# Performance work log

Measured on AMD Instinct MI355X. Metric: run time of the kernel, lower is better.

Reference implementation:

```python
import jax, jax.numpy as jnp
import numpy as np

B, S, D, H, HD = 2, 2048, 2048, 16, 128
MAX_TIMESCALE = 10000.0


def _fixed_pos_embedding(features, length, max_timescale):
    # flaxformer embedding.generate_fixed_pos_embedding
    fraction = jnp.arange(0, features, 2, dtype=jnp.float32) / features
    timescale = max_timescale ** fraction  # min_timescale = 1.0
    sinusoid = jnp.einsum('i,j->ij', jnp.arange(length, dtype=jnp.float32), 1.0 / timescale)
    sinusoid = jnp.concatenate([sinusoid, sinusoid], axis=-1)  # [length, features]
    return jnp.sin(sinusoid), jnp.cos(sinusoid)


def _rotate_half(x):
    x1, x2 = jnp.split(x, 2, axis=-1)
    return jnp.concatenate([-x2, x1], axis=-1)


def _apply_rope(x, sin, cos):
    # x: [B, S, H, HD]; sin/cos: [S, HD]
    sin = sin[None, :, None, :].astype(x.dtype)
    cos = cos[None, :, None, :].astype(x.dtype)
    return x * cos + _rotate_half(x) * sin


def setup_inputs() -> dict:
    key = jax.random.key(0)
    ks = jax.random.split(key, 6)
    inputs_q = jax.random.normal(ks[0], (B, S, D), dtype=jnp.float32)
    inputs_kv = jax.random.normal(ks[1], (B, S, D), dtype=jnp.float32)
    scale = D ** -0.5
    wq = jax.random.normal(ks[2], (D, H, HD), dtype=jnp.float32) * scale
    wk = jax.random.normal(ks[3], (D, H, HD), dtype=jnp.float32) * scale
    wv = jax.random.normal(ks[4], (D, H, HD), dtype=jnp.float32) * scale
    wo = jax.random.normal(ks[5], (H, HD, D), dtype=jnp.float32) * ((H * HD) ** -0.5)
    mask = jnp.tril(jnp.ones((S, S), dtype=bool))[None, None]  # causal [1,1,S,S]
    return {"inputs_q": inputs_q, "inputs_kv": inputs_kv, "wq": wq, "wk": wk,
            "wv": wv, "wo": wo, "mask": mask}


def reference(inputs_q, inputs_kv, wq, wk, wv, wo, mask):
    # QKV projections (split-head kernels) -> [B, S, H, HD]
    q = jnp.einsum('bqd,dhf->bqhf', inputs_q, wq)
    k = jnp.einsum('bkd,dhf->bkhf', inputs_kv, wk)
    v = jnp.einsum('bkd,dhf->bkhf', inputs_kv, wv)

    # Rotary embeddings applied to full head dim (fraction_to_rotate = 1.0)
    sin, cos = _fixed_pos_embedding(HD, S, MAX_TIMESCALE)
    q = _apply_rope(q, sin, cos)
    k = _apply_rope(k, sin, cos)

    # Logit rescaling by 1/sqrt(head_dim) (rescale_logits=False default path)
    q = q * (HD ** -0.5)

    logits = jnp.einsum('bqhf,bkhf->bhqk', q, k)  # [B, H, S, S]
    logits = jnp.where(mask, logits, jnp.asarray(-1e10, logits.dtype))
    probs = jax.nn.softmax(logits, axis=-1)

    ctx = jnp.einsum('bhqk,bkhf->bqhf', probs, v)
    out = jnp.einsum('bqhf,hfd->bqd', ctx, wo)  # output projection
    return out
```

## Files before the change

kernel.cpp:

```cpp
#include <hip/hip_runtime.h>

#define S_LEN 2048
#define NH 16
#define HDIM 128
#define DMODEL 2048

typedef __attribute__((ext_vector_type(8))) short bf16x8;
typedef __attribute__((ext_vector_type(4))) float f32x4;

using gas_cvp = const __attribute__((address_space(1))) void*;
using las_vp  = __attribute__((address_space(3))) void*;

__device__ __forceinline__ unsigned short f2bf(float x) {
  unsigned int u = __builtin_bit_cast(unsigned int, x);
  u += 0x7FFFu + ((u >> 16) & 1u);
  return (unsigned short)(u >> 16);
}
__device__ __forceinline__ float bf2f(unsigned short u) {
  unsigned int x = ((unsigned int)u) << 16;
  return __builtin_bit_cast(float, x);
}
__device__ __forceinline__ unsigned int cvt_pk_bf16(float lo, float hi) {
  unsigned int r;
  asm("v_cvt_pk_bf16_f32 %0, %1, %2" : "=v"(r) : "v"(lo), "v"(hi));
  return r;
}

__global__ __launch_bounds__(256) void cvt_kernel(const float4* __restrict__ in,
                                                  ushort4* __restrict__ out, int n4) {
  int i = blockIdx.x * 256 + threadIdx.x;
  if (i < n4) {
    float4 v = in[i];
    ushort4 r;
    r.x = f2bf(v.x); r.y = f2bf(v.y); r.z = f2bf(v.z); r.w = f2bf(v.w);
    out[i] = r;
  }
}

__global__ __launch_bounds__(256) void sincos_kernel(float2* __restrict__ sc) {
  int i = blockIdx.x * 256 + threadIdx.x;
  int s = i >> 6, j = i & 63;
  float inv_ts = 1.0f / powf(10000.0f, (float)j * (1.0f / 64.0f));
  float ang = (float)s * inv_ts;
  sc[i] = make_float2(sinf(ang), cosf(ang));
}

__global__ __launch_bounds__(256) void rope8_kernel(const unsigned short* __restrict__ X,
                                                    const float2* __restrict__ sc,
                                                    unsigned short* __restrict__ out,
                                                    float scale) {
  int i = blockIdx.x * 256 + threadIdx.x;
  int m = i >> 7;
  int r = i & 127;
  int h = r >> 3, jb = (r & 7) * 8;
  int s = m & (S_LEN - 1);
  size_t base = (size_t)m * DMODEL + h * HDIM + jb;
  int4 x1 = *(const int4*)(X + base);
  int4 x2 = *(const int4*)(X + base + 64);
  const float2* pp = sc + s * 64 + jb;
  int4 o1, o2;
  int* x1w = (int*)&x1; int* x2w = (int*)&x2;
  int* o1w = (int*)&o1; int* o2w = (int*)&o2;
#pragma unroll
  for (int w = 0; w < 4; w++) {
    float a_lo = bf2f((unsigned short)(x1w[w] & 0xffff));
    float a_hi = bf2f((unsigned short)((unsigned int)x1w[w] >> 16));
    float b_lo = bf2f((unsigned short)(x2w[w] & 0xffff));
    float b_hi = bf2f((unsigned short)((unsigned int)x2w[w] >> 16));
    float2 c0 = pp[w * 2], c1 = pp[w * 2 + 1];
    float r1l = (a_lo * c0.y - b_lo * c0.x) * scale;
    float r1h = (a_hi * c1.y - b_hi * c1.x) * scale;
    float r2l = (b_lo * c0.y + a_lo * c0.x) * scale;
    float r2h = (b_hi * c1.y + a_hi * c1.x) * scale;
    o1w[w] = (int)(cvt_pk_bf16(r1l, r1h));
    o2w[w] = (int)(cvt_pk_bf16(r2l, r2h));
  }
  *(int4*)(out + base) = o1;
  *(int4*)(out + base + 64) = o2;
}

__global__ __launch_bounds__(256) void wtrans_kernel(const float* __restrict__ in,
                                                     unsigned short* __restrict__ out) {
  __shared__ float tile[64][65];
  int c0 = blockIdx.x * 64, r0 = blockIdx.y * 64;
  int tx = threadIdx.x & 63, ty = threadIdx.x >> 6;
#pragma unroll
  for (int i = 0; i < 16; i++) {
    int r = ty + i * 4;
    tile[r][tx] = in[(size_t)(r0 + r) * DMODEL + c0 + tx];
  }
  __syncthreads();
#pragma unroll
  for (int i = 0; i < 16; i++) {
    int c = ty + i * 4;
    out[(size_t)(c0 + c) * DMODEL + r0 + tx] = f2bf(tile[tx][c]);
  }
}

__global__ __launch_bounds__(256) void vtrans_kernel(const unsigned short* __restrict__ vf,
                                                     unsigned short* __restrict__ Vt) {
  __shared__ unsigned short tile[64][65];
  int z = blockIdx.z; int b = z >> 4, h = z & 15;
  const unsigned short* I = vf + (size_t)b * S_LEN * DMODEL + h * HDIM;
  unsigned short* O = Vt + (size_t)z * HDIM * S_LEN;
  int s0 = blockIdx.y * 64, f0 = blockIdx.x * 64;
  int tx = threadIdx.x & 63, ty = threadIdx.x >> 6;
#pragma unroll
  for (int i = 0; i < 16; i++) {
    int r = ty + i * 4;
    tile[r][tx] = I[(size_t)(s0 + r) * DMODEL + f0 + tx];
  }
  __syncthreads();
#pragma unroll
  for (int i = 0; i < 16; i++) {
    int c = ty + i * 4;
    O[(size_t)(f0 + c) * S_LEN + s0 + tx] = tile[tx][c];
  }
}

template <bool BF16OUT>
__global__ __launch_bounds__(512) void gemm4_kernel(
    const unsigned short* __restrict__ Aq,
    const unsigned short* __restrict__ Akv,
    const unsigned short* __restrict__ W,
    void* __restrict__ Cb) {
  constexpr int M = 4096, N = 2048, K = 2048, NT = K / 64;
  __shared__ char lds[98304];
  int z = blockIdx.z;
  const unsigned short* A = (z == 0) ? Aq : Akv;
  const unsigned short* Bt = W + (size_t)z * N * K;
  int bm = blockIdx.y * 256, bn = blockIdx.x * 128;
  int tid = threadIdx.x, wave = tid >> 6, lane = tid & 63;
  int lr = lane & 15, lq = lane >> 4;
  int wr = wave >> 1, wc = wave & 1;

  auto STAGE_U = [&](int t, int buf, int which) {
    int k0 = (t & (NT - 1)) * 64;
    const unsigned short* src = (which < 2) ? A : Bt;
    int rbase = (which < 2) ? (bm + which * 128) : bn;
    char* dst0 = lds + buf * 49152 + which * 16384;
#pragma unroll
    for (int i = 0; i < 2; i++) {
      int o = i * 8192 + wave * 1024 + lane * 16;
      int row = o >> 7, colb = o & 127;
      int sc = colb ^ ((row & 7) << 4);
      __builtin_amdgcn_global_load_lds(
          (gas_cvp)(src + (size_t)(rbase + row) * K + k0 + (sc >> 1)),
          (las_vp)(dst0 + i * 8192 + wave * 1024), 16, 0, 0);
    }
  };
  auto LDA = [&](int buf, int m, int kk) -> bf16x8 {
    int row = wr * 64 + m * 16 + lr;
    int half = row >> 7, r = row & 127;
    int byt = r * 128 + (((kk * 4 + lq) ^ (r & 7)) << 4);
    return *(const bf16x8*)(lds + buf * 49152 + half * 16384 + byt);
  };
  auto LDB = [&](int buf, int n, int kk) -> bf16x8 {
    int row = wc * 64 + n * 16 + lr;
    int byt = row * 128 + (((kk * 4 + lq) ^ (row & 7)) << 4);
    return *(const bf16x8*)(lds + buf * 49152 + 32768 + byt);
  };

  f32x4 acc[4][4] = {};
  bf16x8 aA[2][2], bB[4][2];

  auto MFMA_H = [&](int mg) {
#pragma unroll
    for (int kk = 0; kk < 2; kk++)
#pragma unroll
      for (int mm = 0; mm < 2; mm++)
#pragma unroll
        for (int nn = 0; nn < 4; nn++)
          acc[mg * 2 + mm][nn] = __builtin_amdgcn_mfma_f32_16x16x32_bf16(
              aA[mm][kk], bB[nn][kk], acc[mg * 2 + mm][nn], 0, 0, 0);
  };
  auto PHASE_SYNC = [&]() {
    __builtin_amdgcn_s_barrier();
    asm volatile("s_waitcnt lgkmcnt(0)" ::: "memory");
    __builtin_amdgcn_sched_barrier(0);
    __builtin_amdgcn_s_setprio(1);
  };
  auto PHASE_END = [&]() {
    __builtin_amdgcn_s_setprio(0);
    __builtin_amdgcn_s_barrier();
  };

  STAGE_U(0, 0, 0); STAGE_U(0, 0, 1); STAGE_U(0, 0, 2);
  asm volatile("s_waitcnt vmcnt(0)" ::: "memory");
  __builtin_amdgcn_sched_barrier(0);
  __builtin_amdgcn_s_barrier();

  for (int i = 0; i < NT / 2; i++) {
    int T1 = 2 * i + 1, TN = 2 * i + 2;
#pragma unroll
    for (int kk = 0; kk < 2; kk++) {
#pragma unroll
      for (int mm = 0; mm < 2; mm++) aA[mm][kk] = LDA(0, mm, kk);
#pragma unroll
      for (int nn = 0; nn < 4; nn++) bB[nn][kk] = LDB(0, nn, kk);
    }
    STAGE_U(T1, 1, 2); STAGE_U(T1, 1, 0);
    PHASE_SYNC(); MFMA_H(0); PHASE_END();

#pragma unroll
    for (int kk = 0; kk < 2; kk++)
#pragma unroll
      for (int mm = 0; mm < 2; mm++) aA[mm][kk] = LDA(0, 2 + mm, kk);
    STAGE_U(T1, 1, 1); STAGE_U(TN, 0, 2);
    asm volatile("s_waitcnt vmcnt(2)" ::: "memory");
    __builtin_amdgcn_sched_barrier(0);
    PHASE_SYNC(); MFMA_H(1); PHASE_END();

#pragma unroll
    for (int kk = 0; kk < 2; kk++) {
#pragma unroll
      for (int mm = 0; mm < 2; mm++) aA[mm][kk] = LDA(1, mm, kk);
#pragma unroll
      for (int nn = 0; nn < 4; nn++) bB[nn][kk] = LDB(1, nn, kk);
    }
    STAGE_U(TN, 0, 0); STAGE_U(TN, 0, 1);
    PHASE_SYNC(); MFMA_H(0); PHASE_END();

#pragma unroll
    for (int kk = 0; kk < 2; kk++)
#pragma unroll
      for (int mm = 0; mm < 2; mm++) aA[mm][kk] = LDA(1, 2 + mm, kk);
    asm volatile("s_waitcnt vmcnt(0)" ::: "memory");
    __builtin_amdgcn_sched_barrier(0);
    PHASE_SYNC(); MFMA_H(1); PHASE_END();
  }

#pragma unroll
  for (int m = 0; m < 4; m++)
#pragma unroll
    for (int n = 0; n < 4; n++) {
      int row0 = bm + wr * 64 + m * 16 + lq * 4;
      int col = bn + wc * 64 + n * 16 + lr;
      if (BF16OUT) {
        unsigned short* C = (unsigned short*)Cb + (size_t)z * M * N;
#pragma unroll
        for (int r = 0; r < 4; r++)
          C[(size_t)(row0 + r) * N + col] = f2bf(acc[m][n][r]);
      } else {
        float* C = (float*)Cb + (size_t)z * M * N;
#pragma unroll
        for (int r = 0; r < 4; r++)
          C[(size_t)(row0 + r) * N + col] = acc[m][n][r];
      }
    }
}

__global__ __launch_bounds__(512, 1) void attn_kernel(const unsigned short* __restrict__ Qb,
                                                      const unsigned short* __restrict__ Kb,
                                                      const unsigned short* __restrict__ Vt,
                                                      unsigned short* __restrict__ ctx) {
  __shared__ char lds[65536];
  int b = blockIdx.z, h = blockIdx.y;
  int tid = threadIdx.x, wave = tid >> 6, lane = tid & 63;
  int lr = lane & 15, lq = lane >> 4;
  int grp = wave >> 2, wsub = wave & 3;
  int jlo = blockIdx.x;
  int qtile = grp ? (15 - jlo) : jlo;
  int qw = qtile * 128 + wsub * 32;
  int nt = 2 * (15 - jlo) + 2;

  const unsigned short* Qp = Qb + (size_t)b * S_LEN * DMODEL + (size_t)h * HDIM;
  const unsigned short* Kp = Kb + (size_t)b * S_LEN * DMODEL + (size_t)h * HDIM;
  const unsigned short* Vp = Vt + (size_t)(b * NH + h) * HDIM * S_LEN;

  bf16x8 qa[2][4];
#pragma unroll
  for (int mi = 0; mi < 2; mi++)
#pragma unroll
    for (int kf = 0; kf < 4; kf++)
      qa[mi][kf] = *(const bf16x8*)(Qp + (size_t)(qw + mi * 16 + lr) * DMODEL + kf * 32 + lq * 8);

  f32x4 o[2][8] = {};
  float mrow[2] = {-1e30f, -1e30f};
  float lsum[2] = {0.f, 0.f};

  auto STAGE = [&](int tt, int bsel) {
    int kk0 = tt * 64;
#pragma unroll
    for (int i = 0; i < 2; i++) {
      int o_ = wave * 2048 + i * 1024 + lane * 16;
      int row = o_ >> 8, colb = o_ & 255;
      int sc_ = colb ^ ((row & 7) << 4);
      __builtin_amdgcn_global_load_lds(
          (gas_cvp)(Kp + (size_t)(kk0 + row) * DMODEL + (sc_ >> 1)),
          (las_vp)(lds + bsel * 32768 + wave * 2048 + i * 1024), 16, 0, 0);
    }
#pragma unroll
    for (int i = 0; i < 2; i++) {
      int o_ = wave * 2048 + i * 1024 + lane * 16;
      int row = o_ >> 7, colb = o_ & 127;
      int sc_ = colb ^ ((row & 7) << 4);
      __builtin_amdgcn_global_load_lds(
          (gas_cvp)(Vp + (size_t)row * S_LEN + kk0 + (sc_ >> 1)),
          (las_vp)(lds + bsel * 32768 + 16384 + wave * 2048 + i * 1024), 16, 0, 0);
    }
  };

  STAGE(0, 0);
  __syncthreads();

  for (int t = 0; t < nt; t++) {
    int cur = t & 1;
    int k0 = t * 64;
    if (t + 1 < nt) STAGE(t + 1, cur ^ 1);

    bool active = (k0 <= qw + 31);
    if (active) {
      const char* kbb = lds + cur * 32768;
      f32x4 sf[2][4] = {};
#pragma unroll
      for (int kf = 0; kf < 4; kf++) {
        bf16x8 kbf[4];
#pragma unroll
        for (int nf = 0; nf < 4; nf++) {
          int row = nf * 16 + lr;
          int colb = kf * 64 + lq * 16;
          kbf[nf] = *(const bf16x8*)(kbb + row * 256 + (colb ^ ((row & 7) << 4)));
        }
#pragma unroll
        for (int nf = 0; nf < 4; nf++)
#pragma unroll
          for (int mi = 0; mi < 2; mi++)
            sf[mi][nf] = __builtin_amdgcn_mfma_f32_16x16x32_bf16(kbf[nf], qa[mi][kf], sf[mi][nf], 0, 0, 0);
      }

      if (k0 + 63 > qw) {
#pragma unroll
        for (int mi = 0; mi < 2; mi++) {
          int q = qw + mi * 16 + lr;
#pragma unroll
          for (int nf = 0; nf < 4; nf++)
#pragma unroll
            for (int r = 0; r < 4; r++)
              if (k0 + nf * 16 + lq * 4 + r > q) sf[mi][nf][r] = -1e30f;
        }
      }

      float vmax[2];
#pragma unroll
      for (int mi = 0; mi < 2; mi++) {
        float v = sf[mi][0][0];
#pragma unroll
        for (int nf = 0; nf < 4; nf++)
#pragma unroll
          for (int r = 0; r < 4; r++) v = fmaxf(v, sf[mi][nf][r]);
        v = fmaxf(v, __shfl_xor(v, 16));
        v = fmaxf(v, __shfl_xor(v, 32));
        vmax[mi] = v;
      }
      bool need = (vmax[0] > mrow[0] + 8.f) || (vmax[1] > mrow[1] + 8.f);
      if (__any(need)) {
#pragma unroll
        for (int mi = 0; mi < 2; mi++) {
          float mn = fmaxf(mrow[mi], vmax[mi]);
          float al = __expf(mrow[mi] - mn);
          mrow[mi] = mn;
          lsum[mi] *= al;
#pragma unroll
          for (int ff = 0; ff < 8; ff++) o[mi][ff] *= al;
        }
      }
#pragma unroll
      for (int mi = 0; mi < 2; mi++) {
        float rs = 0.f;
#pragma unroll
        for (int nf = 0; nf < 4; nf++)
#pragma unroll
          for (int r = 0; r < 4; r++) {
            float p = __expf(sf[mi][nf][r] - mrow[mi]);
            sf[mi][nf][r] = p;
            rs += p;
          }
        rs += __shfl_xor(rs, 16);
        rs += __shfl_xor(rs, 32);
        lsum[mi] += rs;
      }

      const char* vbb = lds + cur * 32768 + 16384;
      bool hi = (lane >= 32);
      bool odd = (lq & 1);
#pragma unroll
      for (int c = 0; c < 2; c++) {
        bf16x8 pfrag[2];
#pragma unroll
        for (int mi = 0; mi < 2; mi++) {
          unsigned int A0 = cvt_pk_bf16(sf[mi][2 * c][0], sf[mi][2 * c][1]);
          unsigned int A1 = cvt_pk_bf16(sf[mi][2 * c][2], sf[mi][2 * c][3]);
          unsigned int B0 = cvt_pk_bf16(sf[mi][2 * c + 1][0], sf[mi][2 * c + 1][1]);
          unsigned int B1 = cvt_pk_bf16(sf[mi][2 * c + 1][2], sf[mi][2 * c + 1][3]);
          unsigned int sA0 = (unsigned int)__shfl_xor((int)A0, 32);
          unsigned int sA1 = (unsigned int)__shfl_xor((int)A1, 32);
          unsigned int sB0 = (unsigned int)__shfl_xor((int)B0, 32);
          unsigned int sB1 = (unsigned int)__shfl_xor((int)B1, 32);
          unsigned int Y0f = hi ? sB0 : A0, Y0s = hi ? B0 : sA0;
          unsigned int Y1f = hi ? sB1 : A1, Y1s = hi ? B1 : sA1;
          unsigned int z0 = odd ? Y0f : Y0s, z1 = odd ? Y1f : Y1s;
          unsigned int w0 = (unsigned int)__shfl_xor((int)z0, 16);
          unsigned int w1 = (unsigned int)__shfl_xor((int)z1, 16);
          int4 fr;
          fr.x = (int)(odd ? w0 : Y0f);
          fr.y = (int)(odd ? w1 : Y1f);
          fr.z = (int)(odd ? Y0s : w0);
          fr.w = (int)(odd ? Y1s : w1);
          pfrag[mi] = __builtin_bit_cast(bf16x8, fr);
        }
#pragma unroll
        for (int ff = 0; ff < 8; ff++) {
          int row = ff * 16 + lr;
          int colb = c * 64 + lq * 16;
          bf16x8 vb = *(const bf16x8*)(vbb + row * 128 + (colb ^ ((row & 7) << 4)));
#pragma unroll
          for (int mi = 0; mi < 2; mi++)
            o[mi][ff] = __builtin_amdgcn_mfma_f32_16x16x32_bf16(vb, pfrag[mi], o[mi][ff], 0, 0, 0);
        }
      }
    }

    __syncthreads();
  }

#pragma unroll
  for (int mi = 0; mi < 2; mi++) {
    float inv = 1.0f / lsum[mi];
    size_t rb = ((size_t)b * S_LEN + qw + mi * 16 + lr) * DMODEL + h * HDIM;
#pragma unroll
    for (int ff = 0; ff < 8; ff++) {
      unsigned int u0 = cvt_pk_bf16(o[mi][ff][0] * inv, o[mi][ff][1] * inv);
      unsigned int u1 = cvt_pk_bf16(o[mi][ff][2] * inv, o[mi][ff][3] * inv);
      *(uint2*)(ctx + rb + ff * 16 + lq * 4) = make_uint2(u0, u1);
    }
  }
}

extern "C" void kernel_launch(void* const* d_in, const int* in_sizes, int n_in,
                              void* d_out, int out_size, void* d_ws, size_t ws_size,
                              hipStream_t stream) {
  const float* inq  = (const float*)d_in[0];
  const float* inkv = (const float*)d_in[1];
  const float* wq   = (const float*)d_in[2];
  const float* wk   = (const float*)d_in[3];
  const float* wv   = (const float*)d_in[4];
  const float* wo   = (const float*)d_in[5];
  float* out = (float*)d_out;

  char* ws = (char*)d_ws;
  const size_t MB = 1ull << 20;
  unsigned short* xq  = (unsigned short*)(ws);
  unsigned short* xkv = (unsigned short*)(ws + 16 * MB);
  unsigned short* wqt = (unsigned short*)(ws + 32 * MB);
  unsigned short* wkt = (unsigned short*)(ws + 40 * MB);
  unsigned short* wvt = (unsigned short*)(ws + 48 * MB);
  unsigned short* wot = (unsigned short*)(ws + 56 * MB);
  float2* sc          = (float2*)(ws + 64 * MB);
  unsigned short* projb = (unsigned short*)(ws + 66 * MB);
  unsigned short* Vt   = (unsigned short*)(ws + 114 * MB);
  unsigned short* ctxb = (unsigned short*)(ws + 130 * MB);
  unsigned short* Qb = xq;
  unsigned short* Kb = xkv;

  const int n4 = (2 * S_LEN * DMODEL) / 4;
  cvt_kernel<<<n4 / 256, 256, 0, stream>>>((const float4*)inq, (ushort4*)xq, n4);
  cvt_kernel<<<n4 / 256, 256, 0, stream>>>((const float4*)inkv, (ushort4*)xkv, n4);

  dim3 tg(32, 32);
  wtrans_kernel<<<tg, 256, 0, stream>>>(wq, wqt);
  wtrans_kernel<<<tg, 256, 0, stream>>>(wk, wkt);
  wtrans_kernel<<<tg, 256, 0, stream>>>(wv, wvt);
  wtrans_kernel<<<tg, 256, 0, stream>>>(wo, wot);

  sincos_kernel<<<(S_LEN * 64) / 256, 256, 0, stream>>>(sc);

  const float qscale = 0.08838834764831845f;
  unsigned short* projQ = projb;
  unsigned short* projK = projb + (size_t)4096 * 2048;
  unsigned short* projV = projb + (size_t)2 * 4096 * 2048;

  gemm4_kernel<true><<<dim3(16, 16, 3), 512, 0, stream>>>(xq, xkv, wqt, (void*)projb);

  rope8_kernel<<<2048, 256, 0, stream>>>(projQ, sc, Qb, qscale);
  rope8_kernel<<<2048, 256, 0, stream>>>(projK, sc, Kb, 1.0f);
  vtrans_kernel<<<dim3(2, 32, 32), 256, 0, stream>>>(projV, Vt);

  attn_kernel<<<dim3(8, NH, 2), 512, 0, stream>>>(Qb, Kb, Vt, ctxb);

  gemm4_kernel<false><<<dim3(16, 16, 1), 512, 0, stream>>>(ctxb, ctxb, wot, (void*)out);
}
```

Baseline: 299.8 us.

## Triple-buffer GEMM LDS pipeline and remap block order for XCD locality

The GEMM moves from a double-buffered LDS ring to a triple-buffered one (LDS grows from 96KB to 144KB) with two K-tiles prefetched ahead. The loop is rewritten to process one tile per iteration with a rotating buffer index. GEMM and attention blocks are also renumbered so that neighbouring tiles or heads land on the same XCD (the wid&7 style mapping) for better L2 reuse. The aims are to hide more global-load latency and to improve cache locality, at the cost of more LDS per block.

```diff
diff --git a/kernel.cpp b/kernel.cpp
--- a/kernel.cpp
+++ b/kernel.cpp
@@ -119,17 +119,21 @@
 }
 
 template <bool BF16OUT>
-__global__ __launch_bounds__(512) void gemm4_kernel(
+__global__ __launch_bounds__(512) void gemm3b_kernel(
     const unsigned short* __restrict__ Aq,
     const unsigned short* __restrict__ Akv,
     const unsigned short* __restrict__ W,
     void* __restrict__ Cb) {
   constexpr int M = 4096, N = 2048, K = 2048, NT = K / 64;
-  __shared__ char lds[98304];
+  __shared__ char lds[147456];
   int z = blockIdx.z;
   const unsigned short* A = (z == 0) ? Aq : Akv;
   const unsigned short* Bt = W + (size_t)z * N * K;
-  int bm = blockIdx.y * 256, bn = blockIdx.x * 128;
+
+  int wid = blockIdx.y * 16 + blockIdx.x;
+  int nid = (wid & 7) * 32 + (wid >> 3);
+  int bn = (nid & 15) * 128, bm = (nid >> 4) * 256;
+
   int tid = threadIdx.x, wave = tid >> 6, lane = tid & 63;
   int lr = lane & 15, lq = lane >> 4;
   int wr = wave >> 1, wc = wave & 1;
@@ -186,48 +190,35 @@
   };
 
   STAGE_U(0, 0, 0); STAGE_U(0, 0, 1); STAGE_U(0, 0, 2);
-  asm volatile("s_waitcnt vmcnt(0)" ::: "memory");
+  STAGE_U(1, 1, 0); STAGE_U(1, 1, 1); STAGE_U(1, 1, 2);
+  asm volatile("s_waitcnt vmcnt(6)" ::: "memory");
   __builtin_amdgcn_sched_barrier(0);
   __builtin_amdgcn_s_barrier();
 
-  for (int i = 0; i < NT / 2; i++) {
-    int T1 = 2 * i + 1, TN = 2 * i + 2;
+  int cur = 0;
+  for (int T = 0; T < NT; T++) {
+    int t2 = (T + 2) & (NT - 1);
+    int b2 = cur + 2; if (b2 >= 3) b2 -= 3;
 #pragma unroll
     for (int kk = 0; kk < 2; kk++) {
 #pragma unroll
-      for (int mm = 0; mm < 2; mm++) aA[mm][kk] = LDA(0, mm, kk);
-#pragma unroll
-      for (int nn = 0; nn < 4; nn++) bB[nn][kk] = LDB(0, nn, kk);
-    }
-    STAGE_U(T1, 1, 2); STAGE_U(T1, 1, 0);
+      for (int mm = 0; mm < 2; mm++) aA[mm][kk] = LDA(cur, mm, kk);
+#pragma unroll
+      for (int nn = 0; nn < 4; nn++) bB[nn][kk] = LDB(cur, nn, kk);
+    }
+    STAGE_U(t2, b2, 2); STAGE_U(t2, b2, 0);
     PHASE_SYNC(); MFMA_H(0); PHASE_END();
 
 #pragma unroll
     for (int kk = 0; kk < 2; kk++)
 #pragma unroll
-      for (int mm = 0; mm < 2; mm++) aA[mm][kk] = LDA(0, 2 + mm, kk);
-    STAGE_U(T1, 1, 1); STAGE_U(TN, 0, 2);
-    asm volatile("s_waitcnt vmcnt(2)" ::: "memory");
+      for (int mm = 0; mm < 2; mm++) aA[mm][kk] = LDA(cur, 2 + mm, kk);
+    STAGE_U(t2, b2, 1);
+    asm volatile("s_waitcnt vmcnt(6)" ::: "memory");
     __builtin_amdgcn_sched_barrier(0);
     PHASE_SYNC(); MFMA_H(1); PHASE_END();
 
-#pragma unroll
-    for (int kk = 0; kk < 2; kk++) {
-#pragma unroll
-      for (int mm = 0; mm < 2; mm++) aA[mm][kk] = LDA(1, mm, kk);
-#pragma unroll
-      for (int nn = 0; nn < 4; nn++) bB[nn][kk] = LDB(1, nn, kk);
-    }
-    STAGE_U(TN, 0, 0); STAGE_U(TN, 0, 1);
-    PHASE_SYNC(); MFMA_H(0); PHASE_END();
-
-#pragma unroll
-    for (int kk = 0; kk < 2; kk++)
-#pragma unroll
-      for (int mm = 0; mm < 2; mm++) aA[mm][kk] = LDA(1, 2 + mm, kk);
-    asm volatile("s_waitcnt vmcnt(0)" ::: "memory");
-    __builtin_amdgcn_sched_barrier(0);
-    PHASE_SYNC(); MFMA_H(1); PHASE_END();
+    cur++; if (cur == 3) cur = 0;
   }
 
 #pragma unroll
@@ -255,11 +246,14 @@
                                                       const unsigned short* __restrict__ Vt,
                                                       unsigned short* __restrict__ ctx) {
   __shared__ char lds[65536];
-  int b = blockIdx.z, h = blockIdx.y;
+  int d = blockIdx.x + 8 * (blockIdx.y + 16 * blockIdx.z);
+  int jlo = (d >> 3) & 7;
+  int hb = (d & 7) * 4 + (d >> 6);
+  int h = hb & 15, b = hb >> 4;
+
   int tid = threadIdx.x, wave = tid >> 6, lane = tid & 63;
   int lr = lane & 15, lq = lane >> 4;
   int grp = wave >> 2, wsub = wave & 3;
-  int jlo = blockIdx.x;
   int qtile = grp ? (15 - jlo) : jlo;
   int qw = qtile * 128 + wsub * 32;
   int nt = 2 * (15 - jlo) + 2;
@@ -480,7 +474,7 @@
   unsigned short* projK = projb + (size_t)4096 * 2048;
   unsigned short* projV = projb + (size_t)2 * 4096 * 2048;
 
-  gemm4_kernel<true><<<dim3(16, 16, 3), 512, 0, stream>>>(xq, xkv, wqt, (void*)projb);
+  gemm3b_kernel<true><<<dim3(16, 16, 3), 512, 0, stream>>>(xq, xkv, wqt, (void*)projb);
 
   rope8_kernel<<<2048, 256, 0, stream>>>(projQ, sc, Qb, qscale);
   rope8_kernel<<<2048, 256, 0, stream>>>(projK, sc, Kb, 1.0f);
@@ -488,5 +482,5 @@
 
   attn_kernel<<<dim3(8, NH, 2), 512, 0, stream>>>(Qb, Kb, Vt, ctxb);
 
-  gemm4_kernel<false><<<dim3(16, 16, 1), 512, 0, stream>>>(ctxb, ctxb, wot, (void*)out);
-}
+  gemm3b_kernel<false><<<dim3(16, 16, 1), 512, 0, stream>>>(ctxb, ctxb, wot, (void*)out);
+}
```

Measured after the change: 297.4 us. Within noise of the previous version (-0.8%).
